# Optimization experiments

Measured on AMD Instinct MI355X. Metric: run time of the kernel, lower is better.

The kernel has to match this reference:

```python
import jax, jax.numpy as jnp
import numpy as np

CHANNELS = 64
K = 3
STRIDE = 1
GROUP_CHANNELS = 2
GROUPS = CHANNELS // GROUP_CHANNELS  # 32
RED = 4
PAD = (K - 1) // 2


def setup_inputs() -> dict:
    key = jax.random.key(0)
    ks = jax.random.split(key, 6)
    x = jax.random.normal(ks[0], (8, CHANNELS, 128, 128), dtype=jnp.float32)
    w1 = jax.random.normal(ks[1], (CHANNELS // RED, CHANNELS), dtype=jnp.float32) * 0.05
    b1 = jax.random.normal(ks[2], (CHANNELS // RED,), dtype=jnp.float32) * 0.05
    prelu_a = jnp.full((1,), 0.25, dtype=jnp.float32)
    w2 = jax.random.normal(ks[3], (K * K * GROUPS, CHANNELS // RED), dtype=jnp.float32) * 0.05
    b2 = jax.random.normal(ks[4], (K * K * GROUPS,), dtype=jnp.float32) * 0.05
    return {"x": x, "w1": w1, "b1": b1, "prelu_a": prelu_a, "w2": w2, "b2": b2}


def reference(x, w1, b1, prelu_a, w2, b2):
    # stride == 1: no avgpool
    # 1x1 conv -> PReLU -> 1x1 conv to generate per-pixel kernels
    t = jnp.einsum('bchw,oc->bohw', x, w1) + b1[None, :, None, None]
    t = jnp.where(t >= 0, t, prelu_a[0] * t)  # PReLU, single shared slope
    weight = jnp.einsum('bchw,oc->bohw', t, w2) + b2[None, :, None, None]
    b, _, h, w = weight.shape
    # (b, groups, 1, k^2, h, w)
    weight = weight.reshape(b, GROUPS, 1, K * K, h, w)
    # unfold: im2col with padding 1, stride 1; channel-major (c, kh, kw) ordering like torch.nn.Unfold
    xp = jnp.pad(x, ((0, 0), (0, 0), (PAD, PAD), (PAD, PAD)))
    patches = jnp.stack(
        [xp[:, :, i:i + h, j:j + w] for i in range(K) for j in range(K)], axis=2
    )  # (b, c, k^2, h, w)
    patches = patches.reshape(b, GROUPS, GROUP_CHANNELS, K * K, h, w)
    out = (weight * patches).sum(axis=3).reshape(b, CHANNELS, h, w)
    return out
```

## Files before the change

kernel.cpp:

```cpp
#include <hip/hip_runtime.h>

#define NPIX (128 * 128)
#define CH 64
#define RMID 16
#define KK 9
#define TOTPIX (8 * NPIX)

__global__ __launch_bounds__(256) void conv1_kernel(
    const float* __restrict__ x,
    const float* __restrict__ w1,
    const float* __restrict__ b1,
    const float* __restrict__ prelu_a,
    float* __restrict__ t_ws)
{
    __shared__ float pl[2][128][17];

    const int px    = threadIdx.x & 127;
    const int layer = threadIdx.x >> 7;

    const int G  = blockIdx.x * 128 + px;
    const int bq = G >> 14;
    const int p  = G & (NPIX - 1);

    const float* xp = x + (size_t)bq * CH * NPIX + (size_t)(32 * layer) * NPIX + p;

    float xv[32];
#pragma unroll
    for (int c = 0; c < 32; ++c) xv[c] = xp[(size_t)c * NPIX];

    float t[RMID];
#pragma unroll
    for (int r = 0; r < RMID; ++r) t[r] = (layer == 0) ? b1[r] : 0.f;

#pragma unroll
    for (int c = 0; c < 32; ++c) {
#pragma unroll
        for (int r = 0; r < RMID; ++r)
            t[r] = fmaf(w1[r * CH + 32 * layer + c], xv[c], t[r]);
    }
#pragma unroll
    for (int r = 0; r < RMID; ++r) pl[layer][px][r] = t[r];
    __syncthreads();

    const float a  = prelu_a[0];
    const int   r0 = 8 * layer;
#pragma unroll
    for (int r = 0; r < 8; ++r) {
        const float v = pl[0][px][r0 + r] + pl[1][px][r0 + r];
        t_ws[(r0 + r) * TOTPIX + G] = (v >= 0.f) ? v : a * v;
    }
}

__global__ __launch_bounds__(256) void invol_kernel(
    const float* __restrict__ x,
    const float* __restrict__ t_ws,
    const float* __restrict__ w2,
    const float* __restrict__ b2,
    float* __restrict__ out)
{
    const int px   = threadIdx.x & 127;
    const int rsub = threadIdx.x >> 7;

    const int L     = blockIdx.x;
    const int bq    = L & 7;
    const int gq    = (L >> 3) & 7;
    const int strip = L >> 6;

    const int hq = 2 * strip + rsub;
    const int p  = hq * 128 + px;

    const int G = (bq << 14) + p;
    float tr[RMID];
#pragma unroll
    for (int r = 0; r < RMID; ++r) tr[r] = t_ws[r * TOTPIX + G];

    const int   pb   = 4 * p;
    const int   cneg = (px > 0)   ? pb - 4 : pb;
    const int   cpos = (px < 127) ? pb + 4 : pb;
    const float mneg = (px > 0)   ? 1.f : 0.f;
    const float mpos = (px < 127) ? 1.f : 0.f;

    const int   ro0 = (hq > 0)   ? -512 : 0;
    const int   ro2 = (hq < 127) ?  512 : 0;
    const float rm0 = (hq > 0)   ? 1.f : 0.f;
    const float rm2 = (hq < 127) ? 1.f : 0.f;

    const char* xbc = (const char*)(x   + (size_t)bq * CH * NPIX);
    char*       obc = (char*)      (out + (size_t)bq * CH * NPIX);

#pragma unroll 2
    for (int gi = 0; gi < 4; ++gi) {
        const int g = 4 * gq + gi;
        const char* c0 = xbc + (size_t)(2 * g) * NPIX * 4;
        const char* c1 = c0 + NPIX * 4;

        float p0[KK], p1[KK];
#pragma unroll
        for (int i = 0; i < 3; ++i) {
            const int ro = (i == 0) ? ro0 : (i == 2) ? ro2 : 0;
#pragma unroll
            for (int j = 0; j < 3; ++j) {
                const int k    = i * 3 + j;
                const int voff = (j == 0) ? cneg : (j == 2) ? cpos : pb;
                p0[k] = *(const float*)(c0 + (size_t)(voff + ro));
                p1[k] = *(const float*)(c1 + (size_t)(voff + ro));
            }
        }

        float wg[KK];
#pragma unroll
        for (int k = 0; k < KK; ++k) {
            float acc = b2[g * KK + k];
            const float* w2r = w2 + (g * KK + k) * RMID;
#pragma unroll
            for (int r = 0; r < RMID; ++r)
                acc = fmaf(w2r[r], tr[r], acc);
            wg[k] = acc;
        }
        wg[0] *= mneg * rm0;  wg[1] *= rm0;  wg[2] *= mpos * rm0;
        wg[3] *= mneg;                       wg[5] *= mpos;
        wg[6] *= mneg * rm2;  wg[7] *= rm2;  wg[8] *= mpos * rm2;

        float o0 = 0.f, o1 = 0.f;
#pragma unroll
        for (int k = 0; k < KK; ++k) {
            o0 = fmaf(wg[k], p0[k], o0);
            o1 = fmaf(wg[k], p1[k], o1);
        }
        __builtin_nontemporal_store(o0, (float*)(obc + (size_t)(2 * g)     * NPIX * 4 + pb));
        __builtin_nontemporal_store(o1, (float*)(obc + (size_t)(2 * g + 1) * NPIX * 4 + pb));
    }
}

extern "C" void kernel_launch(void* const* d_in, const int* in_sizes, int n_in,
                              void* d_out, int out_size, void* d_ws, size_t ws_size,
                              hipStream_t stream)
{
    const float* x  = (const float*)d_in[0];
    const float* w1 = (const float*)d_in[1];
    const float* b1 = (const float*)d_in[2];
    const float* pa = (const float*)d_in[3];
    const float* w2 = (const float*)d_in[4];
    const float* b2 = (const float*)d_in[5];
    float* out  = (float*)d_out;
    float* t_ws = (float*)d_ws;

    hipLaunchKernelGGL(conv1_kernel, dim3(TOTPIX / 128), dim3(256), 0, stream,
                       x, w1, b1, pa, t_ws);
    hipLaunchKernelGGL(invol_kernel, dim3(8 * 8 * 64), dim3(256), 0, stream,
                       x, t_ws, w2, b2, out);
}
```

Baseline: 130.0 us.

## Process two pixels per thread with packed FMA and shuffle-based halo exchange

Each thread in the involution kernel now handles two adjacent columns, using float2 loads for the intermediate features and input rows. The 16-wide dot product is packed into v2f FMAs so the hardware can use packed-FP32 instructions. Horizontal neighbours come from wavefront shuffles instead of extra unaligned global loads, and the grid is halved to match. This cuts load instructions and ALU issue count, at the cost of shuffle latency, a horizontal reduction per weight, and fewer threads in flight.

```diff
diff --git a/kernel.cpp b/kernel.cpp
--- a/kernel.cpp
+++ b/kernel.cpp
@@ -5,6 +5,9 @@
 #define RMID 16
 #define KK 9
 #define TOTPIX (8 * NPIX)
+#define PLANE_B 65536
+
+typedef float v2f __attribute__((ext_vector_type(2)));
 
 __global__ __launch_bounds__(256) void conv1_kernel(
     const float* __restrict__ x,
@@ -58,77 +61,113 @@
     const float* __restrict__ b2,
     float* __restrict__ out)
 {
-    const int px   = threadIdx.x & 127;
-    const int rsub = threadIdx.x >> 7;
+    const int c    = threadIdx.x & 63;
+    const int rsub = threadIdx.x >> 6;
 
     const int L     = blockIdx.x;
     const int bq    = L & 7;
     const int gq    = (L >> 3) & 7;
     const int strip = L >> 6;
 
-    const int hq = 2 * strip + rsub;
-    const int p  = hq * 128 + px;
+    const int hq   = 4 * strip + rsub;
+    const int col0 = 2 * c;
+    const int p0   = hq * 128 + col0;
 
-    const int G = (bq << 14) + p;
-    float tr[RMID];
+    const int G0 = (bq << 14) + p0;
+    v2f trA[8], trB[8];
 #pragma unroll
-    for (int r = 0; r < RMID; ++r) tr[r] = t_ws[r * TOTPIX + G];
+    for (int i = 0; i < 8; ++i) {
+        const v2f va = *(const v2f*)(t_ws + (size_t)(2 * i)     * TOTPIX + G0);
+        const v2f vb = *(const v2f*)(t_ws + (size_t)(2 * i + 1) * TOTPIX + G0);
+        trA[i].x = va.x; trA[i].y = vb.x;
+        trB[i].x = va.y; trB[i].y = vb.y;
+    }
 
-    const int   pb   = 4 * p;
-    const int   cneg = (px > 0)   ? pb - 4 : pb;
-    const int   cpos = (px < 127) ? pb + 4 : pb;
-    const float mneg = (px > 0)   ? 1.f : 0.f;
-    const float mpos = (px < 127) ? 1.f : 0.f;
-
-    const int   ro0 = (hq > 0)   ? -512 : 0;
-    const int   ro2 = (hq < 127) ?  512 : 0;
     const float rm0 = (hq > 0)   ? 1.f : 0.f;
     const float rm2 = (hq < 127) ? 1.f : 0.f;
+    const float mL  = (c > 0)    ? 1.f : 0.f;
+    const float mR  = (c < 63)   ? 1.f : 0.f;
+    v2f mk[KK];
+#pragma unroll
+    for (int i = 0; i < 3; ++i) {
+        const float rmv = (i == 0) ? rm0 : (i == 2) ? rm2 : 1.f;
+        mk[i * 3 + 0].x = rmv * mL;  mk[i * 3 + 0].y = rmv;
+        mk[i * 3 + 1].x = rmv;       mk[i * 3 + 1].y = rmv;
+        mk[i * 3 + 2].x = rmv;       mk[i * 3 + 2].y = rmv * mR;
+    }
+
+    const int ro0 = (hq > 0)   ? -512 : 0;
+    const int ro2 = (hq < 127) ?  512 : 0;
 
     const char* xbc = (const char*)(x   + (size_t)bq * CH * NPIX);
     char*       obc = (char*)      (out + (size_t)bq * CH * NPIX);
+    const int   pb0 = 4 * p0;
 
-#pragma unroll 2
+#pragma unroll
     for (int gi = 0; gi < 4; ++gi) {
         const int g = 4 * gq + gi;
-        const char* c0 = xbc + (size_t)(2 * g) * NPIX * 4;
-        const char* c1 = c0 + NPIX * 4;
+        const char* c0p = xbc + (size_t)(2 * g) * PLANE_B;
+        const char* c1p = c0p + PLANE_B;
 
-        float p0[KK], p1[KK];
+        const v2f a0 = *(const v2f*)(c0p + (size_t)(pb0 + ro0));
+        const v2f a1 = *(const v2f*)(c0p + (size_t)pb0);
+        const v2f a2 = *(const v2f*)(c0p + (size_t)(pb0 + ro2));
+        const v2f e0 = *(const v2f*)(c1p + (size_t)(pb0 + ro0));
+        const v2f e1 = *(const v2f*)(c1p + (size_t)pb0);
+        const v2f e2 = *(const v2f*)(c1p + (size_t)(pb0 + ro2));
+
+        v2f wgp[KK];
 #pragma unroll
-        for (int i = 0; i < 3; ++i) {
-            const int ro = (i == 0) ? ro0 : (i == 2) ? ro2 : 0;
+        for (int k = 0; k < KK; ++k) {
+            const v2f* w2r2 = (const v2f*)(w2 + (g * KK + k) * RMID);
+            v2f accA, accB;
+            accA.x = b2[g * KK + k]; accA.y = 0.f;
+            accB = accA;
 #pragma unroll
-            for (int j = 0; j < 3; ++j) {
-                const int k    = i * 3 + j;
-                const int voff = (j == 0) ? cneg : (j == 2) ? cpos : pb;
-                p0[k] = *(const float*)(c0 + (size_t)(voff + ro));
-                p1[k] = *(const float*)(c1 + (size_t)(voff + ro));
+            for (int r = 0; r < RMID / 2; ++r) {
+                accA = __builtin_elementwise_fma(w2r2[r], trA[r], accA);
+                accB = __builtin_elementwise_fma(w2r2[r], trB[r], accB);
             }
+            v2f wk;
+            wk.x = accA.x + accA.y;
+            wk.y = accB.x + accB.y;
+            wgp[k] = wk * mk[k];
         }
 
-        float wg[KK];
-#pragma unroll
-        for (int k = 0; k < KK; ++k) {
-            float acc = b2[g * KK + k];
-            const float* w2r = w2 + (g * KK + k) * RMID;
-#pragma unroll
-            for (int r = 0; r < RMID; ++r)
-                acc = fmaf(w2r[r], tr[r], acc);
-            wg[k] = acc;
+        const float lA0 = __shfl_up(a0.y, 1), rA0 = __shfl_down(a0.x, 1);
+        const float lA1 = __shfl_up(a1.y, 1), rA1 = __shfl_down(a1.x, 1);
+        const float lA2 = __shfl_up(a2.y, 1), rA2 = __shfl_down(a2.x, 1);
+        const float lE0 = __shfl_up(e0.y, 1), rE0 = __shfl_down(e0.x, 1);
+        const float lE1 = __shfl_up(e1.y, 1), rE1 = __shfl_down(e1.x, 1);
+        const float lE2 = __shfl_up(e2.y, 1), rE2 = __shfl_down(e2.x, 1);
+
+        v2f oA; oA.x = 0.f; oA.y = 0.f;
+        v2f oB = oA;
+        {
+            v2f tp;
+            tp.x = lA0;  tp.y = a0.x;  oA = __builtin_elementwise_fma(wgp[0], tp, oA);
+                                        oA = __builtin_elementwise_fma(wgp[1], a0, oA);
+            tp.x = a0.y; tp.y = rA0;   oA = __builtin_elementwise_fma(wgp[2], tp, oA);
+            tp.x = lA1;  tp.y = a1.x;  oA = __builtin_elementwise_fma(wgp[3], tp, oA);
+                                        oA = __builtin_elementwise_fma(wgp[4], a1, oA);
+            tp.x = a1.y; tp.y = rA1;   oA = __builtin_elementwise_fma(wgp[5], tp, oA);
+            tp.x = lA2;  tp.y = a2.x;  oA = __builtin_elementwise_fma(wgp[6], tp, oA);
+                                        oA = __builtin_elementwise_fma(wgp[7], a2, oA);
+            tp.x = a2.y; tp.y = rA2;   oA = __builtin_elementwise_fma(wgp[8], tp, oA);
+
+            tp.x = lE0;  tp.y = e0.x;  oB = __builtin_elementwise_fma(wgp[0], tp, oB);
+                                        oB = __builtin_elementwise_fma(wgp[1], e0, oB);
+            tp.x = e0.y; tp.y = rE0;   oB = __builtin_elementwise_fma(wgp[2], tp, oB);
+            tp.x = lE1;  tp.y = e1.x;  oB = __builtin_elementwise_fma(wgp[3], tp, oB);
+                                        oB = __builtin_elementwise_fma(wgp[4], e1, oB);
+            tp.x = e1.y; tp.y = rE1;   oB = __builtin_elementwise_fma(wgp[5], tp, oB);
+            tp.x = lE2;  tp.y = e2.x;  oB = __builtin_elementwise_fma(wgp[6], tp, oB);
+                                        oB = __builtin_elementwise_fma(wgp[7], e2, oB);
+            tp.x = e2.y; tp.y = rE2;   oB = __builtin_elementwise_fma(wgp[8], tp, oB);
         }
-        wg[0] *= mneg * rm0;  wg[1] *= rm0;  wg[2] *= mpos * rm0;
-        wg[3] *= mneg;                       wg[5] *= mpos;
-        wg[6] *= mneg * rm2;  wg[7] *= rm2;  wg[8] *= mpos * rm2;
 
-        float o0 = 0.f, o1 = 0.f;
-#pragma unroll
-        for (int k = 0; k < KK; ++k) {
-            o0 = fmaf(wg[k], p0[k], o0);
-            o1 = fmaf(wg[k], p1[k], o1);
-        }
-        __builtin_nontemporal_store(o0, (float*)(obc + (size_t)(2 * g)     * NPIX * 4 + pb));
-        __builtin_nontemporal_store(o1, (float*)(obc + (size_t)(2 * g + 1) * NPIX * 4 + pb));
+        __builtin_nontemporal_store(oA, (v2f*)(obc + (size_t)(2 * g)     * PLANE_B + pb0));
+        __builtin_nontemporal_store(oB, (v2f*)(obc + (size_t)(2 * g + 1) * PLANE_B + pb0));
     }
 }
 
@@ -147,6 +186,6 @@
 
     hipLaunchKernelGGL(conv1_kernel, dim3(TOTPIX / 128), dim3(256), 0, stream,
                        x, w1, b1, pa, t_ws);
-    hipLaunchKernelGGL(invol_kernel, dim3(8 * 8 * 64), dim3(256), 0, stream,
+    hipLaunchKernelGGL(invol_kernel, dim3(8 * 8 * 32), dim3(256), 0, stream,
                        x, t_ws, w2, b2, out);
 }
```

Result: no change. 128.7 us (-1.0%).
